# Kernel optimization log

Measured on AMD Instinct MI355X. Metric: run time of the kernel, lower is better.

Reference implementation:

```python
import jax, jax.numpy as jnp
import numpy as np

D_MODEL = 2048
N_EXPERTS = 64
TOP_K = 2
AUX_LOSS_COEF = 0.01
ENTROPY_COEF = 0.01


def setup_inputs() -> dict:
    key = jax.random.key(0)
    kx, kw = jax.random.split(key)
    x = jax.random.normal(kx, (4, 4096, D_MODEL), dtype=jnp.float32)
    # nn.Linear(d_model, n_experts, bias=False) weight: [E, D]
    W = jax.random.normal(kw, (N_EXPERTS, D_MODEL), dtype=jnp.float32) * 0.02
    temp = jnp.ones((1,), dtype=jnp.float32)
    return {"x": x, "W": W, "temp": temp}


def reference(x, W, temp):
    B, S, D = x.shape
    E = W.shape[0]
    # gate logits: [B,S,E]
    logits = jnp.einsum("bsd,ed->bse", x, W)
    t = jnp.clip(temp, 0.1, 5.0)  # self.temp.clamp(0.1, 5.0); eval mode -> no noise
    probs = jax.nn.softmax(logits / t, axis=-1)
    expert_probs, expert_indices = jax.lax.top_k(probs, TOP_K)  # [B,S,K]
    # scatter ones at top-k indices -> [B,S,E]
    expert_mask = jax.nn.one_hot(expert_indices, E, dtype=probs.dtype).sum(axis=-2)
    # aux losses
    importance = probs.mean(axis=(0, 1))                 # [E]
    load = expert_mask.sum(axis=(0, 1)) / (B * S + 1e-6)  # [E]
    aux_load_loss = (importance * load).sum() * E * AUX_LOSS_COEF
    token_entropy = -(probs * jnp.log(jnp.clip(probs, 1e-8))).sum(axis=-1).mean()
    router_entropy = token_entropy * ENTROPY_COEF
    return (expert_probs, expert_indices, expert_mask, aux_load_loss, router_entropy)
```

## Files before the change

### kernel.cpp

```cpp
#include <hip/hip_runtime.h>
#include <hip/hip_bf16.h>
#include <math.h>

#define D_MODEL 2048
#define N_EXP   64
#define NTOK    16384
#define NBLK    512
#define NSTG    16

typedef short bf16x8 __attribute__((ext_vector_type(8)));
typedef float f32x16 __attribute__((ext_vector_type(16)));
typedef unsigned int u32;

#define OFF_PROBS 0
#define OFF_IDX   32768
#define OFF_MASK  65536
#define OFF_AUX   1114112
#define OFF_ENT   1114113

#define WF_PS 16384

#define MEMFENCE asm volatile("" ::: "memory")
#define FULLBAR() do { MEMFENCE; __builtin_amdgcn_s_barrier(); MEMFENCE; \
                       __builtin_amdgcn_sched_barrier(0); } while (0)

__device__ __forceinline__ void split3(float xv, u32& h, u32& m, u32& l) {
  u32 xb = __builtin_bit_cast(u32, xv);
  u32 hb = xb & 0xFFFF0000u;
  float tf = xv - __builtin_bit_cast(float, hb);
  u32 tb = __builtin_bit_cast(u32, tf);
  u32 mb = tb & 0xFFFF0000u;
  float t2 = tf - __builtin_bit_cast(float, mb);
  u32 lb = __builtin_bit_cast(u32, t2);
  h = hb >> 16; m = mb >> 16; l = lb >> 16;
}

__device__ __forceinline__ bool better(float a, int ia, float b, int ib) {
  return (a > b) || (a == b && ia < ib);
}

__global__ __launch_bounds__(256) void wprep_kernel(
    const float* __restrict__ W, bf16x8* __restrict__ Wf) {
  int gid  = blockIdx.x * 256 + threadIdx.x;
  int g    = gid >> 7;
  int n    = (gid >> 6) & 1;
  int lane = gid & 63;
  int e    = n * 32 + (lane & 31);
  int k    = g * 16 + ((lane >> 5) << 3);
  const float* wr = W + (size_t)e * D_MODEL + k;
  bf16x8 hv, mv, lv;
#pragma unroll
  for (int j = 0; j < 8; ++j) {
    u32 h, m, l;
    split3(wr[j], h, m, l);
    hv[j] = (short)h; mv[j] = (short)m; lv[j] = (short)l;
  }
  Wf[gid]             = hv;
  Wf[WF_PS + gid]     = mv;
  Wf[2 * WF_PS + gid] = lv;
}

__global__ __launch_bounds__(512, 4) void fused_kernel(
    const float* __restrict__ x, const bf16x8* __restrict__ Wf,
    const float* __restrict__ temp, float* __restrict__ out,
    float* __restrict__ imp_part, float* __restrict__ load_part,
    float* __restrict__ ent_part) {
  __shared__ float lds[16384];
  const int tid  = threadIdx.x;
  const int w    = tid >> 6;
  const int lane = tid & 63;
  const int t0   = blockIdx.x * 32;
  const int rl   = lane & 31;
  const int hg   = lane >> 5;

  float tv = temp[0];
  tv = fminf(fmaxf(tv, 0.1f), 5.0f);
  const float invT = 1.0f / tv;

  const float* gsrc[2];
#pragma unroll
  for (int i = 0; i < 2; ++i) {
    int r0  = w * 4 + i * 2;
    int row = r0 + hg;
    int sc  = rl ^ (row & 31);
    gsrc[i] = x + (size_t)(t0 + row) * D_MODEL + sc * 4;
  }

  auto stage = [&](int st) {
    const int buf = st & 3;
#pragma unroll
    for (int i = 0; i < 2; ++i) {
      int r0 = w * 4 + i * 2;
      __builtin_amdgcn_global_load_lds(
          (const __attribute__((address_space(1))) void*)(gsrc[i] + st * 128),
          (__attribute__((address_space(3))) void*)(lds + buf * 4096 + r0 * 128),
          16, 0, 0);
    }
  };
  auto loadB = [&](int st, bf16x8* bb) {
    const bf16x8* wp = Wf + (size_t)(st * 8 + w) * 128 + lane;
#pragma unroll
    for (int p = 0; p < 3; ++p)
#pragma unroll
      for (int n = 0; n < 2; ++n)
        bb[p * 2 + n] = wp[p * WF_PS + n * 64];
  };

  f32x16 acc0, acc1;
#pragma unroll
  for (int i = 0; i < 16; ++i) { acc0[i] = 0.0f; acc1[i] = 0.0f; }

  bf16x8 b[2][6];
  stage(0); stage(1);
  loadB(0, b[0]);
  asm volatile("s_waitcnt vmcnt(8)" ::: "memory");
  FULLBAR();

  const int c0 = w * 4 + hg * 2;

#pragma unroll
  for (int st = 0; st < NSTG; ++st) {
    if (st + 1 < NSTG) loadB(st + 1, b[(st + 1) & 1]);
    if (st + 2 < NSTG) stage(st + 2);

    const float* rb = lds + (st & 3) * 4096 + rl * 128;
    float4 a0 = *(const float4*)(rb + ((c0 ^ rl) << 2));
    float4 a1 = *(const float4*)(rb + (((c0 + 1) ^ rl) << 2));
    float av[8] = {a0.x, a0.y, a0.z, a0.w, a1.x, a1.y, a1.z, a1.w};
    bf16x8 ah, am, al;
#pragma unroll
    for (int j = 0; j < 8; ++j) {
      u32 hh, mm, ll;
      split3(av[j], hh, mm, ll);
      ah[j] = (short)hh; am[j] = (short)mm; al[j] = (short)ll;
    }
    const bf16x8* bb = b[st & 1];
    acc0 = __builtin_amdgcn_mfma_f32_32x32x16_bf16(ah, bb[0], acc0, 0, 0, 0);
    acc1 = __builtin_amdgcn_mfma_f32_32x32x16_bf16(ah, bb[1], acc1, 0, 0, 0);
    acc0 = __builtin_amdgcn_mfma_f32_32x32x16_bf16(ah, bb[2], acc0, 0, 0, 0);
    acc1 = __builtin_amdgcn_mfma_f32_32x32x16_bf16(ah, bb[3], acc1, 0, 0, 0);
    acc0 = __builtin_amdgcn_mfma_f32_32x32x16_bf16(am, bb[0], acc0, 0, 0, 0);
    acc1 = __builtin_amdgcn_mfma_f32_32x32x16_bf16(am, bb[1], acc1, 0, 0, 0);
    acc0 = __builtin_amdgcn_mfma_f32_32x32x16_bf16(am, bb[2], acc0, 0, 0, 0);
    acc1 = __builtin_amdgcn_mfma_f32_32x32x16_bf16(am, bb[3], acc1, 0, 0, 0);
    acc0 = __builtin_amdgcn_mfma_f32_32x32x16_bf16(ah, bb[4], acc0, 0, 0, 0);
    acc1 = __builtin_amdgcn_mfma_f32_32x32x16_bf16(ah, bb[5], acc1, 0, 0, 0);
    acc0 = __builtin_amdgcn_mfma_f32_32x32x16_bf16(al, bb[0], acc0, 0, 0, 0);
    acc1 = __builtin_amdgcn_mfma_f32_32x32x16_bf16(al, bb[1], acc1, 0, 0, 0);

    if (st < NSTG - 2) {
      asm volatile("s_waitcnt vmcnt(8)" ::: "memory");
      FULLBAR();
    } else if (st == NSTG - 2) {
      asm volatile("s_waitcnt vmcnt(6)" ::: "memory");
      FULLBAR();
    }
  }

  __syncthreads();
#pragma unroll
  for (int r = 0; r < 16; ++r) {
    int row = (r & 3) + ((r >> 2) << 3) + (hg << 2);
    lds[w * 2048 + row * 64 + rl]      = acc0[r];
    lds[w * 2048 + row * 64 + 32 + rl] = acc1[r];
  }
  __syncthreads();

  const int row  = tid >> 4;
  const int colq = tid & 15;
  float l0 = 0.f, l1 = 0.f, l2 = 0.f, l3 = 0.f;
  for (int wv = 0; wv < 8; ++wv) {
    float4 v = *(const float4*)&lds[wv * 2048 + row * 64 + colq * 4];
    l0 += v.x; l1 += v.y; l2 += v.z; l3 += v.w;
  }
  l0 *= invT; l1 *= invT; l2 *= invT; l3 *= invT;

  float m = fmaxf(fmaxf(l0, l1), fmaxf(l2, l3));
#pragma unroll
  for (int d = 1; d < 16; d <<= 1) m = fmaxf(m, __shfl_xor(m, d));

  float ls0 = l0 - m, ls1 = l1 - m, ls2 = l2 - m, ls3 = l3 - m;
  float e0 = __expf(ls0), e1 = __expf(ls1), e2 = __expf(ls2), e3 = __expf(ls3);
  float ssum = e0 + e1 + e2 + e3;
  float dot  = e0 * ls0 + e1 * ls1 + e2 * ls2 + e3 * ls3;
#pragma unroll
  for (int d = 1; d < 16; d <<= 1) {
    ssum += __shfl_xor(ssum, d);
    dot  += __shfl_xor(dot, d);
  }
  const float inv_s = 1.0f / ssum;
  const float ent = __logf(ssum) - dot * inv_s;

  const int eb = colq * 4;
  float b1 = e0, b2 = -1.0f;
  int   i1 = eb, i2 = eb + 1;
  {
    float ev[3] = {e1, e2, e3};
#pragma unroll
    for (int j = 0; j < 3; ++j) {
      int ej = eb + 1 + j;
      if (better(ev[j], ej, b1, i1)) { b2 = b1; i2 = i1; b1 = ev[j]; i1 = ej; }
      else if (better(ev[j], ej, b2, i2)) { b2 = ev[j]; i2 = ej; }
    }
  }
#pragma unroll
  for (int d = 1; d < 16; d <<= 1) {
    float ob1 = __shfl_xor(b1, d), ob2 = __shfl_xor(b2, d);
    int   oi1 = __shfl_xor(i1, d), oi2 = __shfl_xor(i2, d);
    if (better(ob1, oi1, b1, i1)) {
      if (better(b1, i1, ob2, oi2)) { b2 = b1; i2 = i1; }
      else                          { b2 = ob2; i2 = oi2; }
      b1 = ob1; i1 = oi1;
    } else if (better(ob1, oi1, b2, i2)) {
      b2 = ob1; i2 = oi1;
    }
  }

  const int t = t0 + row;
  if (colq == 0) {
    out[OFF_PROBS + (size_t)t * 2 + 0] = b1 * inv_s;
    out[OFF_PROBS + (size_t)t * 2 + 1] = b2 * inv_s;
    out[OFF_IDX   + (size_t)t * 2 + 0] = (float)i1;
    out[OFF_IDX   + (size_t)t * 2 + 1] = (float)i2;
  }
  {
    float4 mv;
    mv.x = ((eb + 0 == i1) || (eb + 0 == i2)) ? 1.0f : 0.0f;
    mv.y = ((eb + 1 == i1) || (eb + 1 == i2)) ? 1.0f : 0.0f;
    mv.z = ((eb + 2 == i1) || (eb + 2 == i2)) ? 1.0f : 0.0f;
    mv.w = ((eb + 3 == i1) || (eb + 3 == i2)) ? 1.0f : 0.0f;
    *(float4*)&out[OFF_MASK + (size_t)t * N_EXP + eb] = mv;
  }

  __syncthreads();
  {
    float4 p4;
    p4.x = e0 * inv_s; p4.y = e1 * inv_s; p4.z = e2 * inv_s; p4.w = e3 * inv_s;
    *(float4*)&lds[row * 64 + eb] = p4;
  }
  if (colq == 0) {
    lds[2048 + row] = (float)i1;
    lds[2080 + row] = (float)i2;
    lds[2112 + row] = ent;
  }
  __syncthreads();
  if (tid < 64) {
    float simp = 0.0f, sld = 0.0f;
    const float fe = (float)tid;
    for (int r = 0; r < 32; ++r) simp += lds[r * 64 + tid];
    for (int r = 0; r < 32; ++r)
      sld += ((lds[2048 + r] == fe) ? 1.0f : 0.0f)
           + ((lds[2080 + r] == fe) ? 1.0f : 0.0f);
    imp_part[blockIdx.x * N_EXP + tid]  = simp;
    load_part[blockIdx.x * N_EXP + tid] = sld;
    float v = (tid < 32) ? lds[2112 + tid] : 0.0f;
#pragma unroll
    for (int d = 1; d < 64; d <<= 1) v += __shfl_xor(v, d);
    if (tid == 0) ent_part[blockIdx.x] = v;
  }
}

__global__ __launch_bounds__(256) void finalize_kernel(
    const float* __restrict__ imp_part, const float* __restrict__ load_part,
    const float* __restrict__ ent_part, float* __restrict__ out) {
  __shared__ float simp[4][64], sld[4][64], sent[4];
  const int tid  = threadIdx.x;
  const int lane = tid & 63;
  const int q    = tid >> 6;
  float a = 0.0f, b = 0.0f;
  for (int blk = q * 128; blk < q * 128 + 128; ++blk) {
    a += imp_part[blk * N_EXP + lane];
    b += load_part[blk * N_EXP + lane];
  }
  simp[q][lane] = a;
  sld[q][lane]  = b;
  float e = ent_part[tid] + ent_part[tid + 256];
#pragma unroll
  for (int d = 1; d < 64; d <<= 1) e += __shfl_xor(e, d);
  if (lane == 0) sent[q] = e;
  __syncthreads();
  if (tid < 64) {
    float imp = simp[0][tid] + simp[1][tid] + simp[2][tid] + simp[3][tid];
    float ld  = sld[0][tid] + sld[1][tid] + sld[2][tid] + sld[3][tid];
    imp *= (1.0f / 16384.0f);
    ld  *= (1.0f / (16384.0f + 1e-6f));
    float prod = imp * ld;
#pragma unroll
    for (int d = 1; d < 64; d <<= 1) prod += __shfl_xor(prod, d);
    if (tid == 0) {
      float ent = sent[0] + sent[1] + sent[2] + sent[3];
      out[OFF_AUX] = prod * 64.0f * 0.01f;
      out[OFF_ENT] = (ent / 16384.0f) * 0.01f;
    }
  }
}

extern "C" void kernel_launch(void* const* d_in, const int* in_sizes, int n_in,
                              void* d_out, int out_size, void* d_ws, size_t ws_size,
                              hipStream_t stream) {
  const float* x    = (const float*)d_in[0];
  const float* W    = (const float*)d_in[1];
  const float* temp = (const float*)d_in[2];
  float* out = (float*)d_out;
  float* ws  = (float*)d_ws;

  bf16x8* Wf   = (bf16x8*)ws;
  float*  imp  = ws + 196608;
  float*  ldp  = imp + NBLK * N_EXP;
  float*  entp = ldp + NBLK * N_EXP;

  wprep_kernel<<<64, 256, 0, stream>>>(W, Wf);
  fused_kernel<<<NBLK, 512, 0, stream>>>(x, Wf, temp, out, imp, ldp, entp);
  finalize_kernel<<<1, 256, 0, stream>>>(imp, ldp, entp, out);
}
```

Baseline: 51.98 us.

## Stage x in 256-column super-stages with double buffering and half the barriers

```diff
diff --git a/kernel.cpp b/kernel.cpp
--- a/kernel.cpp
+++ b/kernel.cpp
@@ -7,6 +7,7 @@
 #define NTOK    16384
 #define NBLK    512
 #define NSTG    16
+#define NSUP    8
 
 typedef short bf16x8 __attribute__((ext_vector_type(8)));
 typedef float f32x16 __attribute__((ext_vector_type(16)));
@@ -77,23 +78,21 @@
   tv = fminf(fmaxf(tv, 0.1f), 5.0f);
   const float invT = 1.0f / tv;
 
-  const float* gsrc[2];
-#pragma unroll
-  for (int i = 0; i < 2; ++i) {
-    int r0  = w * 4 + i * 2;
-    int row = r0 + hg;
-    int sc  = rl ^ (row & 31);
-    gsrc[i] = x + (size_t)(t0 + row) * D_MODEL + sc * 4;
-  }
-
-  auto stage = [&](int st) {
-    const int buf = st & 3;
-#pragma unroll
-    for (int i = 0; i < 2; ++i) {
-      int r0 = w * 4 + i * 2;
+  const float* gsrc[4];
+#pragma unroll
+  for (int i = 0; i < 4; ++i) {
+    int r = w * 4 + i;
+    gsrc[i] = x + (size_t)(t0 + r) * D_MODEL + ((lane ^ (r & 7)) << 2);
+  }
+
+  auto stage = [&](int s) {
+    const int buf = s & 1;
+#pragma unroll
+    for (int i = 0; i < 4; ++i) {
+      int r = w * 4 + i;
       __builtin_amdgcn_global_load_lds(
-          (const __attribute__((address_space(1))) void*)(gsrc[i] + st * 128),
-          (__attribute__((address_space(3))) void*)(lds + buf * 4096 + r0 * 128),
+          (const __attribute__((address_space(1))) void*)(gsrc[i] + s * 256),
+          (__attribute__((address_space(3))) void*)(lds + buf * 8192 + r * 256),
           16, 0, 0);
     }
   };
@@ -111,21 +110,21 @@
   for (int i = 0; i < 16; ++i) { acc0[i] = 0.0f; acc1[i] = 0.0f; }
 
   bf16x8 b[2][6];
-  stage(0); stage(1);
+  stage(0);
   loadB(0, b[0]);
-  asm volatile("s_waitcnt vmcnt(8)" ::: "memory");
+  asm volatile("s_waitcnt vmcnt(6)" ::: "memory");
   FULLBAR();
 
-  const int c0 = w * 4 + hg * 2;
-
 #pragma unroll
   for (int st = 0; st < NSTG; ++st) {
+    if ((st & 1) == 0 && (st >> 1) + 1 < NSUP) stage((st >> 1) + 1);
     if (st + 1 < NSTG) loadB(st + 1, b[(st + 1) & 1]);
-    if (st + 2 < NSTG) stage(st + 2);
-
-    const float* rb = lds + (st & 3) * 4096 + rl * 128;
-    float4 a0 = *(const float4*)(rb + ((c0 ^ rl) << 2));
-    float4 a1 = *(const float4*)(rb + (((c0 + 1) ^ rl) << 2));
+
+    const float* rb = lds + ((st >> 1) & 1) * 8192 + rl * 256;
+    const int c = (st & 1) * 32 + w * 4 + hg * 2;
+    const int q = rl & 7;
+    float4 a0 = *(const float4*)(rb + ((c ^ q) << 2));
+    float4 a1 = *(const float4*)(rb + (((c + 1) ^ q) << 2));
     float av[8] = {a0.x, a0.y, a0.z, a0.w, a1.x, a1.y, a1.z, a1.w};
     bf16x8 ah, am, al;
 #pragma unroll
@@ -148,11 +147,8 @@
     acc0 = __builtin_amdgcn_mfma_f32_32x32x16_bf16(al, bb[0], acc0, 0, 0, 0);
     acc1 = __builtin_amdgcn_mfma_f32_32x32x16_bf16(al, bb[1], acc1, 0, 0, 0);
 
-    if (st < NSTG - 2) {
-      asm volatile("s_waitcnt vmcnt(8)" ::: "memory");
-      FULLBAR();
-    } else if (st == NSTG - 2) {
-      asm volatile("s_waitcnt vmcnt(6)" ::: "memory");
+    if ((st & 1) && st < NSTG - 1) {
+      asm volatile("s_waitcnt vmcnt(12)" ::: "memory");
       FULLBAR();
     }
   }
```

After: 59.04 us. +13.6%, slower.
